# Kernel tuning notes

Hardware: AMD Instinct MI355X
Metric: run time of the kernel (lower is better)

Reference implementation:

```python
import math
import jax, jax.numpy as jnp
import numpy as np

B, S, D, H = 2, 2048, 1024, 16
DH = D // H


def setup_inputs() -> dict:
    key = jax.random.key(0)
    ks = jax.random.split(key, 12)
    s = 1.0 / math.sqrt(D)
    return {
        "x_q": jax.random.normal(ks[0], (B, S, D), jnp.float32),
        "x_k": jax.random.normal(ks[1], (B, S, D), jnp.float32),
        "x_v": jax.random.normal(ks[2], (B, S, D), jnp.float32),
        "mask": jax.random.randint(ks[3], (B, S), 0, 2) > 0,
        "Wq": jax.random.normal(ks[4], (D, D), jnp.float32) * s,
        "bq": jnp.zeros((D,), jnp.float32),
        "Wk": jax.random.normal(ks[5], (D, D), jnp.float32) * s,
        "bk": jnp.zeros((D,), jnp.float32),
        "Wv": jax.random.normal(ks[6], (D, D), jnp.float32) * s,
        "bv": jnp.zeros((D,), jnp.float32),
        "Wo": jax.random.normal(ks[7], (D, D), jnp.float32) * s,
        "bo": jnp.zeros((D,), jnp.float32),
    }


def reference(x_q, x_k, x_v, mask, Wq, bq, Wk, bk, Wv, bv, Wo, bo):
    # nn.Linear: y = x @ W^T + b
    Q = jnp.einsum('bsd,ed->bse', x_q, Wq) + bq
    K = jnp.einsum('bsd,ed->bse', x_k, Wk) + bk
    V = jnp.einsum('bsd,ed->bse', x_v, Wv) + bv
    b, sq, d = Q.shape
    # split(dim_split, 2) + cat(dim=0) == per-head attention on [B,S,H,DH]
    Qh = Q.reshape(b, sq, H, DH)
    Kh = K.reshape(b, -1, H, DH)
    Vh = V.reshape(b, -1, H, DH)
    scores = jnp.einsum('bqhd,bkhd->bhqk', Qh, Kh) / math.sqrt(DH)
    # inf_mask: -1e9 where mask is False, broadcast over heads and queries
    scores = scores + jnp.where(mask[:, None, None, :], 0.0, -1e9)
    A = jax.nn.softmax(scores, axis=-1)  # dropout is identity in eval
    out = jnp.einsum('bhqk,bkhd->bqhd', A, Vh).reshape(b, sq, d)
    return jnp.einsum('bsd,ed->bse', out, Wo) + bo
```

## Files before the change

### kernel.cpp

```cpp
#include <hip/hip_runtime.h>
#include <hip/hip_bf16.h>
#include <stdint.h>

#define BB  2
#define SS  2048
#define DDIM 1024
#define HH  16
#define DH  64

typedef __attribute__((ext_vector_type(8))) short short8;
typedef __attribute__((ext_vector_type(4))) short short4v;
typedef __attribute__((ext_vector_type(4))) float float4v;

#define AS1 __attribute__((address_space(1)))
#define AS3 __attribute__((address_space(3)))

static __device__ __forceinline__ void gl2lds16(const void* g, void* l) {
  __builtin_amdgcn_global_load_lds((const AS1 unsigned int*)g,
                                   (AS3 unsigned int*)l, 16, 0, 0);
}

static __device__ __forceinline__ float bf2f(short s) {
  union { unsigned u; float f; } c;
  c.u = ((unsigned)(unsigned short)s) << 16;
  return c.f;
}
static __device__ __forceinline__ short f2bf(float f) {
  union { float ff; unsigned u; } c;
  c.ff = f;
  unsigned u = c.u;
  u += 0x7fffu + ((u >> 16) & 1u);
  return (short)(u >> 16);
}

#if __has_builtin(__builtin_amdgcn_exp2f)
static __device__ __forceinline__ float exp2fast(float x) { return __builtin_amdgcn_exp2f(x); }
#else
static __device__ __forceinline__ float exp2fast(float x) { return __expf(x * 0.69314718056f); }
#endif

static __device__ __forceinline__ unsigned packbf(float x, float y) {
  unsigned ax = __float_as_uint(x) + 0x8000u;
  unsigned ay = __float_as_uint(y) + 0x8000u;
#if __has_builtin(__builtin_amdgcn_perm)
  return __builtin_amdgcn_perm(ay, ax, 0x07060302u);
#else
  return (ax >> 16) | (ay & 0xffff0000u);
#endif
}

static __device__ __forceinline__ int detect_f32(const void* p) {
  const float* f = (const float*)p;
  int ok = 1;
#pragma unroll
  for (int i = 0; i < 16; i++) {
    float a = fabsf(f[i]);
    ok &= (a > 1e-10f && a < 1e4f) ? 1 : 0;
  }
  return ok;
}

struct CvtArgs {
  const void* xq; const void* xk; const void* xv;
  const void* wq; const void* wk; const void* wv; const void* wo;
  const void* b0; const void* b1; const void* b2; const void* b3;
  const int* mask;
  short* dst;
  float* mw;
};

__global__ __launch_bounds__(256)
void cvt_kernel(CvtArgs a) {
  const int f32m = detect_f32(a.xq);
  const size_t gtid = (size_t)blockIdx.x * blockDim.x + threadIdx.x;
  const size_t stride = (size_t)gridDim.x * blockDim.x;
  const size_t M4 = (size_t)4 << 20, M1 = (size_t)1 << 20, TOT = (size_t)16 << 20;
  for (size_t i = gtid; i * 4 < TOT; i += stride) {
    const size_t idx = i * 4;
    const void* src;
    size_t off;
    if (idx < 3 * M4) {
      size_t xi = idx / M4;
      off = idx & (M4 - 1);
      src = (xi == 0) ? a.xq : (xi == 1) ? a.xk : a.xv;
    } else {
      size_t wi = (idx - 3 * M4) / M1;
      off = idx & (M1 - 1);
      src = (wi == 0) ? a.wq : (wi == 1) ? a.wk : (wi == 2) ? a.wv : a.wo;
    }
    short4v o;
    if (f32m) {
      float4v v = *(const float4v*)((const float*)src + off);
#pragma unroll
      for (int j = 0; j < 4; j++) o[j] = f2bf(v[j]);
    } else {
      o = *(const short4v*)((const short*)src + off);
    }
    *(short4v*)(a.dst + idx) = o;
  }
  if (gtid < 1024) {
    const void* bs[4] = {a.b0, a.b1, a.b2, a.b3};
#pragma unroll
    for (int j = 0; j < 4; j++) {
      short v = f32m ? f2bf(((const float*)bs[j])[gtid])
                     : ((const short*)bs[j])[gtid];
      a.dst[TOT + (size_t)j * 1024 + gtid] = v;
    }
  }
  if (gtid < BB * SS)
    a.mw[gtid] = a.mask[gtid] ? -23.083120654223414f : -1e9f;
}

struct GemmArgs {
  const short* x[3];
  const short* w[3];
  const short* b[3];
  short* o[3];
  const void* probe;
  int tmask;
  int detect_out;
};

__global__ __launch_bounds__(256)
void gemm_kernel(GemmArgs a) {
  constexpr int GK = 1024, GN = 1024;
  __shared__ alignas(16) short As[128 * 32];
  __shared__ alignas(16) short Bs[128 * 32];

  const int t = threadIdx.x;
  const int w = t >> 6, l = t & 63, l15 = l & 15, qd = l >> 4;
  const int bn = blockIdx.x, bm = blockIdx.y, mat = blockIdx.z;

  const short* X  = a.x[mat];
  const short* W  = a.w[mat];
  const short* Bi = a.b[mat];
  short* O        = a.o[mat];
  const int transposed = (a.tmask >> mat) & 1;

  const short* Ag = X + (size_t)bm * 128 * GK;
  const short* Bg = W + (size_t)bn * 128 * GK;

  const int L0 = t, L1 = 256 + t;
  const int r0 = L0 >> 2, g0 = (L0 & 3) ^ ((r0 >> 1) & 3);
  const int r1 = L1 >> 2, g1 = (L1 & 3) ^ ((r1 >> 1) & 3);
  const size_t off0 = (size_t)r0 * GK + g0 * 8;
  const size_t off1 = (size_t)r1 * GK + g1 * 8;

  float4v acc[4][4];
#pragma unroll
  for (int i = 0; i < 4; i++)
#pragma unroll
    for (int j = 0; j < 4; j++) acc[i][j] = (float4v){0.f, 0.f, 0.f, 0.f};

  const int wm = (w >> 1) * 64, wn = (w & 1) * 64;

  for (int k0 = 0; k0 < GK; k0 += 32) {
    gl2lds16(Ag + off0 + k0, (char*)As + L0 * 16);
    gl2lds16(Ag + off1 + k0, (char*)As + L1 * 16);
    gl2lds16(Bg + off0 + k0, (char*)Bs + L0 * 16);
    gl2lds16(Bg + off1 + k0, (char*)Bs + L1 * 16);
    __syncthreads();

    short8 af[4], bf[4];
#pragma unroll
    for (int i = 0; i < 4; i++) {
      int m = wm + i * 16 + l15;
      af[i] = *(const short8*)((const char*)As + (m * 4 + (qd ^ ((m >> 1) & 3))) * 16);
      int n = wn + i * 16 + l15;
      bf[i] = *(const short8*)((const char*)Bs + (n * 4 + (qd ^ ((n >> 1) & 3))) * 16);
    }
#pragma unroll
    for (int i = 0; i < 4; i++)
#pragma unroll
      for (int j = 0; j < 4; j++)
        acc[i][j] = __builtin_amdgcn_mfma_f32_16x16x32_bf16(af[i], bf[j], acc[i][j], 0, 0, 0);
    __syncthreads();
  }

  if (!transposed) {
    const int outf32 = a.detect_out ? detect_f32(a.probe) : 0;
    float bj[4];
#pragma unroll
    for (int j = 0; j < 4; j++) bj[j] = bf2f(Bi[bn * 128 + wn + j * 16 + l15]);
#pragma unroll
    for (int i = 0; i < 4; i++) {
      int mgl = bm * 128 + wm + i * 16 + qd * 4;
#pragma unroll
      for (int j = 0; j < 4; j++) {
        int ngl = bn * 128 + wn + j * 16 + l15;
        if (outf32) {
          float* Of = (float*)O;
#pragma unroll
          for (int r = 0; r < 4; r++)
            Of[(size_t)(mgl + r) * GN + ngl] = acc[i][j][r] + bj[j];
        } else {
#pragma unroll
          for (int r = 0; r < 4; r++)
            O[(size_t)(mgl + r) * GN + ngl] = f2bf(acc[i][j][r] + bj[j]);
        }
      }
    }
  } else {
#pragma unroll
    for (int j = 0; j < 4; j++) {
      int ngl = bn * 128 + wn + j * 16 + l15;
      float bb = bf2f(Bi[ngl]);
#pragma unroll
      for (int i = 0; i < 4; i++) {
        int mgl = bm * 128 + wm + i * 16 + qd * 4;
        int bidx = mgl >> 11;
        int s = mgl & (SS - 1);
        short4v v;
#pragma unroll
        for (int r = 0; r < 4; r++) v[r] = f2bf(acc[i][j][r] + bb);
        *(short4v*)(O + (size_t)bidx * DDIM * SS + (size_t)ngl * SS + s) = v;
      }
    }
  }
}

__global__ __launch_bounds__(256)
void flash_kernel(const short* __restrict__ Q, const short* __restrict__ K,
                  const short* __restrict__ Vt, const float* __restrict__ Mw,
                  short* __restrict__ At) {
  __shared__ alignas(16) short Ks[2][64 * 64];
  __shared__ alignas(16) short Vs[2][64 * 64];
  __shared__ alignas(16) float madd[2][64];

  const int t = threadIdx.x;
  const int w = t >> 6, l = t & 63, l15 = l & 15, qd = l >> 4;
  const int bh = blockIdx.x, qt = blockIdx.y;
  const int b = bh >> 4, h = bh & 15;
  const int q0 = qt * 128 + w * 32;

  const float SC = 0.125f * 1.44269504f;

  short8 qf[2][2];
#pragma unroll
  for (int g = 0; g < 2; g++) {
    const short* Qb = Q + ((size_t)(b * SS + q0 + 16 * g + l15)) * DDIM + h * 64;
#pragma unroll
    for (int c = 0; c < 2; c++) qf[g][c] = *(const short8*)(Qb + 32 * c + 8 * qd);
  }

  const short ov = (l15 == 0) ? (short)0x3F80 : (short)0;
  const short8 onesf = {ov, ov, ov, ov, ov, ov, ov, ov};

  const int kr = t >> 3;
  const short* Kg = K + ((size_t)(b * SS + kr)) * DDIM + h * 64
                    + ((t & 7) ^ (kr & 7)) * 8;
  const int vr = t >> 3;
  const short* Vg = Vt + (size_t)b * DDIM * SS + (size_t)(h * 64 + vr) * SS
                    + ((t & 7) ^ (vr & 7)) * 8;
  const float* MwB = Mw + b * SS;

  float4v oacc[2][4], oaccl[2];
#pragma unroll
  for (int g = 0; g < 2; g++) {
    oaccl[g] = (float4v){0.f, 0.f, 0.f, 0.f};
#pragma unroll
    for (int mt = 0; mt < 4; mt++) oacc[g][mt] = (float4v){0.f, 0.f, 0.f, 0.f};
  }

  const int swz = l15 & 7;

  gl2lds16(Kg, (char*)Ks[0] + t * 16);
  gl2lds16(Kg + (size_t)32 * DDIM, (char*)Ks[0] + 4096 + t * 16);
  gl2lds16(Vg, (char*)Vs[0] + t * 16);
  gl2lds16(Vg + 32 * SS, (char*)Vs[0] + 4096 + t * 16);
  float mwN = 0.f;
  if (t < 64) {
    madd[0][t] = MwB[t];
    mwN = MwB[64 + t];
  }

  for (int i = 0; i < 32; i++) {
    const int cur = i & 1, nxt = cur ^ 1;
    asm volatile("s_waitcnt vmcnt(0) lgkmcnt(0)\n\ts_barrier" ::: "memory");

    if (i < 31) {
      const size_t ko = (size_t)((i + 1) * 64) * DDIM;
      gl2lds16(Kg + ko, (char*)Ks[nxt] + t * 16);
      gl2lds16(Kg + ko + (size_t)32 * DDIM, (char*)Ks[nxt] + 4096 + t * 16);
      const int vo = (i + 1) * 64;
      gl2lds16(Vg + vo, (char*)Vs[nxt] + t * 16);
      gl2lds16(Vg + vo + 32 * SS, (char*)Vs[nxt] + 4096 + t * 16);
    }
    if (t < 64) {
      madd[nxt][t] = mwN;
      int idx = (i + 2) * 64 + t;
      if (idx > SS - 1) idx = SS - 1;
      mwN = MwB[idx];
    }

    const short* ksb = Ks[cur];
    const short* vsb = Vs[cur];

    float4v sacc[2][4];
#pragma unroll
    for (int g = 0; g < 2; g++)
#pragma unroll
      for (int mt = 0; mt < 4; mt++) sacc[g][mt] = (float4v){0.f, 0.f, 0.f, 0.f};
#pragma unroll
    for (int mt = 0; mt < 4; mt++) {
#pragma unroll
      for (int c = 0; c < 2; c++) {
        short8 kf = *(const short8*)(ksb + (mt * 16 + l15) * 64 + (((4 * c + qd) ^ swz) * 8));
#pragma unroll
        for (int g = 0; g < 2; g++)
          sacc[g][mt] = __builtin_amdgcn_mfma_f32_16x16x32_bf16(kf, qf[g][c], sacc[g][mt], 0, 0, 0);
      }
    }

    float4v ma[4];
#pragma unroll
    for (int mt = 0; mt < 4; mt++)
      ma[mt] = *(const float4v*)(&madd[cur][16 * mt + 4 * qd]);

#pragma unroll
    for (int pp = 0; pp < 2; pp++) {
      union { short4v h[2]; short8 v8; } vf[4];
#pragma unroll
      for (int mt = 0; mt < 4; mt++) {
        const short* vrp = vsb + (mt * 16 + l15) * 64;
        const int u0 = 8 * pp + qd, u1 = 8 * pp + 4 + qd;
        vf[mt].h[0] = *(const short4v*)(vrp + (((u0 >> 1) ^ swz) * 8) + (u0 & 1) * 4);
        vf[mt].h[1] = *(const short4v*)(vrp + (((u1 >> 1) ^ swz) * 8) + (u1 & 1) * 4);
      }
#pragma unroll
      for (int g = 0; g < 2; g++) {
        float p0[4], p1[4];
#pragma unroll
        for (int r = 0; r < 4; r++) {
          p0[r] = exp2fast(fmaf(sacc[g][2 * pp][r],     SC, ma[2 * pp][r]));
          p1[r] = exp2fast(fmaf(sacc[g][2 * pp + 1][r], SC, ma[2 * pp + 1][r]));
        }
        union { unsigned u[4]; short8 v8; } pk;
        pk.u[0] = packbf(p0[0], p0[1]);
        pk.u[1] = packbf(p0[2], p0[3]);
        pk.u[2] = packbf(p1[0], p1[1]);
        pk.u[3] = packbf(p1[2], p1[3]);
#pragma unroll
        for (int mt = 0; mt < 4; mt++)
          oacc[g][mt] = __builtin_amdgcn_mfma_f32_16x16x32_bf16(vf[mt].v8, pk.v8, oacc[g][mt], 0, 0, 0);
        oaccl[g] = __builtin_amdgcn_mfma_f32_16x16x32_bf16(onesf, pk.v8, oaccl[g], 0, 0, 0);
      }
    }
  }

#pragma unroll
  for (int g = 0; g < 2; g++) {
    const float lg = __shfl(oaccl[g][0], l15);
    const float inv = 1.f / lg;
    short* Og = At + ((size_t)(b * SS + q0 + 16 * g + l15)) * DDIM + h * 64;
#pragma unroll
    for (int mt = 0; mt < 4; mt++) {
      short4v v;
#pragma unroll
      for (int r = 0; r < 4; r++) v[r] = f2bf(oacc[g][mt][r] * inv);
      *(short4v*)(Og + mt * 16 + qd * 4) = v;
    }
  }
}

extern "C" void kernel_launch(void* const* d_in, const int* in_sizes, int n_in,
                              void* d_out, int out_size, void* d_ws, size_t ws_size,
                              hipStream_t stream) {
  (void)in_sizes; (void)n_in; (void)out_size; (void)ws_size;
  const int* mask = (const int*)d_in[3];

  char* ws = (char*)d_ws;
  short* wsBF = (short*)ws;
  const size_t M1 = (size_t)1 << 20;
  short* Qb = (short*)(ws + (size_t)34 * M1);
  short* Kb = (short*)(ws + (size_t)42 * M1);
  short* Vt = (short*)(ws + (size_t)50 * M1);
  short* At = (short*)(ws + (size_t)58 * M1);
  float* Mw = (float*)(ws + (size_t)66 * M1);

  CvtArgs c;
  c.xq = d_in[0]; c.xk = d_in[1]; c.xv = d_in[2];
  c.wq = d_in[4]; c.wk = d_in[6]; c.wv = d_in[8]; c.wo = d_in[10];
  c.b0 = d_in[5]; c.b1 = d_in[7]; c.b2 = d_in[9]; c.b3 = d_in[11];
  c.mask = mask; c.dst = wsBF; c.mw = Mw;
  hipLaunchKernelGGL(cvt_kernel, dim3(4096), dim3(256), 0, stream, c);

  GemmArgs a1;
  a1.x[0] = wsBF;            a1.x[1] = wsBF + 4 * M1;  a1.x[2] = wsBF + 8 * M1;
  a1.w[0] = wsBF + 12 * M1;  a1.w[1] = wsBF + 13 * M1; a1.w[2] = wsBF + 14 * M1;
  a1.b[0] = wsBF + 16 * M1;  a1.b[1] = wsBF + 16 * M1 + 1024;
  a1.b[2] = wsBF + 16 * M1 + 2048;
  a1.o[0] = Qb; a1.o[1] = Kb; a1.o[2] = Vt;
  a1.probe = d_in[0];
  a1.tmask = 4;
  a1.detect_out = 0;
  hipLaunchKernelGGL(gemm_kernel, dim3(8, 32, 3), dim3(256), 0, stream, a1);

  hipLaunchKernelGGL(flash_kernel, dim3(32, 16), dim3(256), 0, stream,
                     Qb, Kb, Vt, Mw, At);

  GemmArgs a2;
  a2.x[0] = At;             a2.w[0] = wsBF + 15 * M1;
  a2.b[0] = wsBF + 16 * M1 + 3072;
  a2.o[0] = (short*)d_out;
  a2.x[1] = a2.x[2] = At; a2.w[1] = a2.w[2] = a2.w[0];
  a2.b[1] = a2.b[2] = a2.b[0]; a2.o[1] = a2.o[2] = a2.o[0];
  a2.probe = d_in[0];
  a2.tmask = 0;
  a2.detect_out = 1;
  hipLaunchKernelGGL(gemm_kernel, dim3(8, 32, 1), dim3(256), 0, stream, a2);
}
```

Before: 245.9 us.

## Template GEMM tile height, permute K rows for vector V loads, use hardware bf16 pack

```diff
diff --git a/kernel.cpp b/kernel.cpp
--- a/kernel.cpp
+++ b/kernel.cpp
@@ -33,21 +33,17 @@
   return (short)(u >> 16);
 }
 
+static __device__ __forceinline__ unsigned cvtpk(float x, float y) {
+  union { __hip_bfloat162 h; unsigned u; } c;
+  c.h = __float22bfloat162_rn(float2{x, y});
+  return c.u;
+}
+
 #if __has_builtin(__builtin_amdgcn_exp2f)
 static __device__ __forceinline__ float exp2fast(float x) { return __builtin_amdgcn_exp2f(x); }
 #else
 static __device__ __forceinline__ float exp2fast(float x) { return __expf(x * 0.69314718056f); }
 #endif
-
-static __device__ __forceinline__ unsigned packbf(float x, float y) {
-  unsigned ax = __float_as_uint(x) + 0x8000u;
-  unsigned ay = __float_as_uint(y) + 0x8000u;
-#if __has_builtin(__builtin_amdgcn_perm)
-  return __builtin_amdgcn_perm(ay, ax, 0x07060302u);
-#else
-  return (ax >> 16) | (ay & 0xffff0000u);
-#endif
-}
 
 static __device__ __forceinline__ int detect_f32(const void* p) {
   const float* f = (const float*)p;
@@ -91,8 +87,10 @@
     short4v o;
     if (f32m) {
       float4v v = *(const float4v*)((const float*)src + off);
-#pragma unroll
-      for (int j = 0; j < 4; j++) o[j] = f2bf(v[j]);
+      union { unsigned u[2]; short4v s; } pk;
+      pk.u[0] = cvtpk(v[0], v[1]);
+      pk.u[1] = cvtpk(v[2], v[3]);
+      o = pk.s;
     } else {
       o = *(const short4v*)((const short*)src + off);
     }
@@ -121,10 +119,11 @@
   int detect_out;
 };
 
+template <int MW>
 __global__ __launch_bounds__(256)
 void gemm_kernel(GemmArgs a) {
   constexpr int GK = 1024, GN = 1024;
-  __shared__ alignas(16) short As[128 * 32];
+  __shared__ alignas(16) short As[32 * MW * 32];
   __shared__ alignas(16) short Bs[128 * 32];
 
   const int t = threadIdx.x;
@@ -137,7 +136,7 @@
   short* O        = a.o[mat];
   const int transposed = (a.tmask >> mat) & 1;
 
-  const short* Ag = X + (size_t)bm * 128 * GK;
+  const short* Ag = X + (size_t)bm * (32 * MW) * GK;
   const short* Bg = W + (size_t)bn * 128 * GK;
 
   const int L0 = t, L1 = 256 + t;
@@ -146,31 +145,34 @@
   const size_t off0 = (size_t)r0 * GK + g0 * 8;
   const size_t off1 = (size_t)r1 * GK + g1 * 8;
 
-  float4v acc[4][4];
-#pragma unroll
-  for (int i = 0; i < 4; i++)
+  float4v acc[MW][4];
+#pragma unroll
+  for (int i = 0; i < MW; i++)
 #pragma unroll
     for (int j = 0; j < 4; j++) acc[i][j] = (float4v){0.f, 0.f, 0.f, 0.f};
 
-  const int wm = (w >> 1) * 64, wn = (w & 1) * 64;
+  const int wm = (w >> 1) * 16 * MW, wn = (w & 1) * 64;
 
   for (int k0 = 0; k0 < GK; k0 += 32) {
     gl2lds16(Ag + off0 + k0, (char*)As + L0 * 16);
-    gl2lds16(Ag + off1 + k0, (char*)As + L1 * 16);
+    if (MW == 4) gl2lds16(Ag + off1 + k0, (char*)As + L1 * 16);
     gl2lds16(Bg + off0 + k0, (char*)Bs + L0 * 16);
     gl2lds16(Bg + off1 + k0, (char*)Bs + L1 * 16);
     __syncthreads();
 
-    short8 af[4], bf[4];
-#pragma unroll
-    for (int i = 0; i < 4; i++) {
+    short8 af[MW], bf[4];
+#pragma unroll
+    for (int i = 0; i < MW; i++) {
       int m = wm + i * 16 + l15;
       af[i] = *(const short8*)((const char*)As + (m * 4 + (qd ^ ((m >> 1) & 3))) * 16);
-      int n = wn + i * 16 + l15;
-      bf[i] = *(const short8*)((const char*)Bs + (n * 4 + (qd ^ ((n >> 1) & 3))) * 16);
-    }
-#pragma unroll
-    for (int i = 0; i < 4; i++)
+    }
+#pragma unroll
+    for (int j = 0; j < 4; j++) {
+      int n = wn + j * 16 + l15;
+      bf[j] = *(const short8*)((const char*)Bs + (n * 4 + (qd ^ ((n >> 1) & 3))) * 16);
+    }
+#pragma unroll
+    for (int i = 0; i < MW; i++)
 #pragma unroll
       for (int j = 0; j < 4; j++)
         acc[i][j] = __builtin_amdgcn_mfma_f32_16x16x32_bf16(af[i], bf[j], acc[i][j], 0, 0, 0);
@@ -183,8 +185,8 @@
 #pragma unroll
     for (int j = 0; j < 4; j++) bj[j] = bf2f(Bi[bn * 128 + wn + j * 16 + l15]);
 #pragma unroll
-    for (int i = 0; i < 4; i++) {
-      int mgl = bm * 128 + wm + i * 16 + qd * 4;
+    for (int i = 0; i < MW; i++) {
+      int mgl = bm * (32 * MW) + wm + i * 16 + qd * 4;
 #pragma unroll
       for (int j = 0; j < 4; j++) {
         int ngl = bn * 128 + wn + j * 16 + l15;
@@ -206,8 +208,8 @@
       int ngl = bn * 128 + wn + j * 16 + l15;
       float bb = bf2f(Bi[ngl]);
 #pragma unroll
-      for (int i = 0; i < 4; i++) {
-        int mgl = bm * 128 + wm + i * 16 + qd * 4;
+      for (int i = 0; i < MW; i++) {
+        int mgl = bm * (32 * MW) + wm + i * 16 + qd * 4;
         int bidx = mgl >> 11;
         int s = mgl & (SS - 1);
         short4v v;
@@ -247,7 +249,8 @@
   const short8 onesf = {ov, ov, ov, ov, ov, ov, ov, ov};
 
   const int kr = t >> 3;
-  const short* Kg = K + ((size_t)(b * SS + kr)) * DDIM + h * 64
+  const int pkr = ((kr & 12) << 1) | ((kr & 16) >> 2) | (kr & 3);
+  const short* Kg = K + ((size_t)(b * SS + pkr)) * DDIM + h * 64
                     + ((t & 7) ^ (kr & 7)) * 8;
   const int vr = t >> 3;
   const short* Vg = Vt + (size_t)b * DDIM * SS + (size_t)(h * 64 + vr) * SS
@@ -312,37 +315,30 @@
       }
     }
 
-    float4v ma[4];
-#pragma unroll
-    for (int mt = 0; mt < 4; mt++)
-      ma[mt] = *(const float4v*)(&madd[cur][16 * mt + 4 * qd]);
-
 #pragma unroll
     for (int pp = 0; pp < 2; pp++) {
-      union { short4v h[2]; short8 v8; } vf[4];
-#pragma unroll
-      for (int mt = 0; mt < 4; mt++) {
-        const short* vrp = vsb + (mt * 16 + l15) * 64;
-        const int u0 = 8 * pp + qd, u1 = 8 * pp + 4 + qd;
-        vf[mt].h[0] = *(const short4v*)(vrp + (((u0 >> 1) ^ swz) * 8) + (u0 & 1) * 4);
-        vf[mt].h[1] = *(const short4v*)(vrp + (((u1 >> 1) ^ swz) * 8) + (u1 & 1) * 4);
-      }
+      float4v ma0 = *(const float4v*)(&madd[cur][32 * pp + 8 * qd]);
+      float4v ma1 = *(const float4v*)(&madd[cur][32 * pp + 8 * qd + 4]);
+      short8 vf[4];
+#pragma unroll
+      for (int mt = 0; mt < 4; mt++)
+        vf[mt] = *(const short8*)(vsb + (mt * 16 + l15) * 64 + (((4 * pp + qd) ^ swz) * 8));
 #pragma unroll
       for (int g = 0; g < 2; g++) {
         float p0[4], p1[4];
 #pragma unroll
         for (int r = 0; r < 4; r++) {
-          p0[r] = exp2fast(fmaf(sacc[g][2 * pp][r],     SC, ma[2 * pp][r]));
-          p1[r] = exp2fast(fmaf(sacc[g][2 * pp + 1][r], SC, ma[2 * pp + 1][r]));
+          p0[r] = exp2fast(fmaf(sacc[g][2 * pp][r],     SC, ma0[r]));
+          p1[r] = exp2fast(fmaf(sacc[g][2 * pp + 1][r], SC, ma1[r]));
         }
         union { unsigned u[4]; short8 v8; } pk;
-        pk.u[0] = packbf(p0[0], p0[1]);
-        pk.u[1] = packbf(p0[2], p0[3]);
-        pk.u[2] = packbf(p1[0], p1[1]);
-        pk.u[3] = packbf(p1[2], p1[3]);
+        pk.u[0] = cvtpk(p0[0], p0[1]);
+        pk.u[1] = cvtpk(p0[2], p0[3]);
+        pk.u[2] = cvtpk(p1[0], p1[1]);
+        pk.u[3] = cvtpk(p1[2], p1[3]);
 #pragma unroll
         for (int mt = 0; mt < 4; mt++)
-          oacc[g][mt] = __builtin_amdgcn_mfma_f32_16x16x32_bf16(vf[mt].v8, pk.v8, oacc[g][mt], 0, 0, 0);
+          oacc[g][mt] = __builtin_amdgcn_mfma_f32_16x16x32_bf16(vf[mt], pk.v8, oacc[g][mt], 0, 0, 0);
         oaccl[g] = __builtin_amdgcn_mfma_f32_16x16x32_bf16(onesf, pk.v8, oaccl[g], 0, 0, 0);
       }
     }
@@ -394,7 +390,8 @@
   a1.probe = d_in[0];
   a1.tmask = 4;
   a1.detect_out = 0;
-  hipLaunchKernelGGL(gemm_kernel, dim3(8, 32, 3), dim3(256), 0, stream, a1);
+  hipLaunchKernelGGL(HIP_KERNEL_NAME(gemm_kernel<4>), dim3(8, 32, 3), dim3(256),
+                     0, stream, a1);
 
   hipLaunchKernelGGL(flash_kernel, dim3(32, 16), dim3(256), 0, stream,
                      Qb, Kb, Vt, Mw, At);
@@ -408,5 +405,6 @@
   a2.probe = d_in[0];
   a2.tmask = 0;
   a2.detect_out = 1;
-  hipLaunchKernelGGL(gemm_kernel, dim3(8, 32, 1), dim3(256), 0, stream, a2);
-}
+  hipLaunchKernelGGL(HIP_KERNEL_NAME(gemm_kernel<2>), dim3(8, 64, 1), dim3(256),
+                     0, stream, a2);
+}
```

New measurement: 239.7 us. 1.03x faster.
